# Kernel tuning notes

Hardware: AMD Instinct MI355X
Metric: run time of the kernel (lower is better)

Reference implementation:

```python
import jax, jax.numpy as jnp
import numpy as np
import math

# Config: 8 packed images, each a 32x32 patch grid (t=1) -> equal seglen 1024
NSEG, GH, GW = 8, 32, 32
L = GH * GW            # 1024 tokens per segment
S = NSEG * L           # 8192 packed tokens
H, NH = 1024, 16
HD = H // NH           # 64, head dim (rope dim), divisible by 4
MLP = 4096
THETA = 10000.0


def _make_rope_cos_sin():
    # Rope2DPosEmb._precompute_freqs_cis for a (GH, GW) grid, dim=HD
    flat = np.arange(L, dtype=np.float32)
    x_pos = flat % GW
    y_pos = flat // GW
    dim_range = np.arange(0, HD, 4, dtype=np.float32)[: HD // 4]
    freqs = 1.0 / THETA ** (dim_range / HD)          # [HD//4]
    x_f = np.outer(x_pos, freqs)                     # [L, HD//4]
    y_f = np.outer(y_pos, freqs)
    # interleave x/y angles per frequency -> [L, HD//2]
    ang = np.stack([x_f, y_f], axis=-1).reshape(L, HD // 2)
    ang = np.tile(ang, (NSEG, 1))                    # same grid repeated per image
    return jnp.asarray(np.cos(ang)), jnp.asarray(np.sin(ang))


def setup_inputs() -> dict:
    key = jax.random.key(0)
    ks = jax.random.split(key, 8)
    cos, sin = _make_rope_cos_sin()
    inp = {
        "x": jax.random.normal(ks[0], (S, H), jnp.float32),
        "wqkv": jax.random.normal(ks[1], (3 * H, H), jnp.float32) * math.sqrt(1.0 / H),
        "wo": jax.random.normal(ks[2], (H, H), jnp.float32) * math.sqrt(1.0 / H),
        "ln0_g": jnp.ones((H,), jnp.float32),
        "ln0_b": jnp.zeros((H,), jnp.float32),
        "ln1_g": jnp.ones((H,), jnp.float32),
        "ln1_b": jnp.zeros((H,), jnp.float32),
        "fc0_w": jax.random.normal(ks[3], (MLP, H), jnp.float32) * math.sqrt(2.0 / H),
        "fc0_b": jnp.zeros((MLP,), jnp.float32),
        "fc1_w": jax.random.normal(ks[4], (H, MLP), jnp.float32) * math.sqrt(2.0 / MLP),
        "fc1_b": jnp.zeros((H,), jnp.float32),
        "rope_cos": cos,
        "rope_sin": sin,
        "cu_seqlens": jnp.arange(NSEG + 1, dtype=jnp.int32) * L,
    }
    return inp


def _layernorm(x, g, b, eps=1e-5):
    m = x.mean(-1, keepdims=True)
    v = ((x - m) ** 2).mean(-1, keepdims=True)
    return (x - m) * jax.lax.rsqrt(v + eps) * g + b


def _apply_rope(x, cos, sin):
    # x: [S, NH, HD]; cos/sin: [S, HD//2]. Complex mult on (even, odd) pairs.
    xr = x.reshape(S, NH, HD // 2, 2)
    x0, x1 = xr[..., 0], xr[..., 1]
    c = cos[:, None, :]
    s = sin[:, None, :]
    o0 = x0 * c - x1 * s
    o1 = x0 * s + x1 * c
    return jnp.stack([o0, o1], axis=-1).reshape(S, NH, HD)


def reference(x, wqkv, wo, ln0_g, ln0_b, ln1_g, ln1_b,
              fc0_w, fc0_b, fc1_w, fc1_b, rope_cos, rope_sin, cu_seqlens):
    # --- attention branch (pre-norm) ---
    h = _layernorm(x, ln0_g, ln0_b)
    qkv = (h @ wqkv.T).reshape(S, 3, NH, HD)
    q, k, v = qkv[:, 0], qkv[:, 1], qkv[:, 2]
    q = _apply_rope(q, rope_cos, rope_sin)
    k = _apply_rope(k, rope_cos, rope_sin)
    # block-diagonal varlen attention: equal-length segments -> reshape
    qb = q.reshape(NSEG, L, NH, HD)
    kb = k.reshape(NSEG, L, NH, HD)
    vb = v.reshape(NSEG, L, NH, HD)
    scores = jnp.einsum("blhd,bmhd->bhlm", qb, kb) / math.sqrt(HD)
    p = jax.nn.softmax(scores.astype(jnp.float32), axis=-1).astype(x.dtype)
    attn = jnp.einsum("bhlm,bmhd->blhd", p, vb).reshape(S, H)
    x = x + attn @ wo.T
    # --- MLP branch (pre-norm) ---
    h2 = _layernorm(x, ln1_g, ln1_b)
    mlp = jax.nn.gelu(h2 @ fc0_w.T + fc0_b, approximate=False) @ fc1_w.T + fc1_b
    return x + mlp
```

## Files before the change

kernel.cpp:

```cpp
#include <hip/hip_runtime.h>
#include <math.h>


typedef __bf16 bf16x8 __attribute__((ext_vector_type(8)));
typedef float f32x4 __attribute__((ext_vector_type(4)));
typedef float f32x16 __attribute__((ext_vector_type(16)));
typedef unsigned int u32;

__device__ __forceinline__ unsigned short f2b(float f) {
  unsigned u = __float_as_uint(f);
  return (unsigned short)((u + 0x7FFFu + ((u >> 16) & 1u)) >> 16);
}
__device__ __forceinline__ float b2f(unsigned short h) {
  return __uint_as_float(((unsigned)h) << 16);
}
__device__ __forceinline__ void async_ld16(const void* g, void* l) {
  __builtin_amdgcn_global_load_lds((__attribute__((address_space(1))) void*)g,
                                   (__attribute__((address_space(3))) void*)l,
                                   16, 0, 0);
}
__device__ __forceinline__ float exp2fast(float x) {
#if __has_builtin(__builtin_amdgcn_exp2f)
  return __builtin_amdgcn_exp2f(x);
#else
  return exp2f(x);
#endif
}
__device__ __forceinline__ float rcpfast(float x) {
#if __has_builtin(__builtin_amdgcn_rcpf)
  return __builtin_amdgcn_rcpf(x);
#else
  return 1.0f / x;
#endif
}

__global__ __launch_bounds__(256) void castln_kernel(
    const float* __restrict__ w0, const float* __restrict__ w1,
    const float* __restrict__ w2, const float* __restrict__ w3,
    unsigned short* __restrict__ wdst,
    const float* __restrict__ x, const float* __restrict__ g,
    const float* __restrict__ bt, unsigned short* __restrict__ hout) {
  __shared__ float red[8];
  const int blk = blockIdx.x;
  if (blk < 12288) {
    const int t = blk * 256 + threadIdx.x;
    const float* src;
    int off;
    if (t < 786432) { src = w0; off = t; }
    else if (t < 1048576) { src = w1; off = t - 786432; }
    else if (t < 2097152) { src = w2; off = t - 1048576; }
    else { src = w3; off = t - 2097152; }
    const float4 v = ((const float4*)src)[off];
    ushort4 o;
    o.x = f2b(v.x); o.y = f2b(v.y); o.z = f2b(v.z); o.w = f2b(v.w);
    ((ushort4*)wdst)[t] = o;
    return;
  }
  const int row = blk - 12288, t = threadIdx.x;
  const float4 v = ((const float4*)(x + (size_t)row * 1024))[t];
  float s = v.x + v.y + v.z + v.w;
  float s2 = v.x * v.x + v.y * v.y + v.z * v.z + v.w * v.w;
#pragma unroll
  for (int m = 1; m < 64; m <<= 1) {
    s += __shfl_xor(s, m, 64);
    s2 += __shfl_xor(s2, m, 64);
  }
  if ((t & 63) == 0) { red[t >> 6] = s; red[4 + (t >> 6)] = s2; }
  __syncthreads();
  const float ts = red[0] + red[1] + red[2] + red[3];
  const float ts2 = red[4] + red[5] + red[6] + red[7];
  const float mean = ts * (1.f / 1024.f);
  const float var = ts2 * (1.f / 1024.f) - mean * mean;
  const float inv = rsqrtf(var + 1e-5f);
  const float4 gv = ((const float4*)g)[t];
  const float4 bv = ((const float4*)bt)[t];
  ushort4 o;
  o.x = f2b((v.x - mean) * inv * gv.x + bv.x);
  o.y = f2b((v.y - mean) * inv * gv.y + bv.y);
  o.z = f2b((v.z - mean) * inv * gv.z + bv.z);
  o.w = f2b((v.w - mean) * inv * gv.w + bv.w);
  ((ushort4*)hout)[(size_t)row * 256 + t] = o;
}

__global__ __launch_bounds__(256) void ln_kernel(const float* __restrict__ x,
                                                 const float* __restrict__ g,
                                                 const float* __restrict__ bt,
                                                 unsigned short* __restrict__ out) {
  __shared__ float red[8];
  const int row = blockIdx.x, t = threadIdx.x;
  const float4 v = ((const float4*)(x + (size_t)row * 1024))[t];
  float s = v.x + v.y + v.z + v.w;
  float s2 = v.x * v.x + v.y * v.y + v.z * v.z + v.w * v.w;
#pragma unroll
  for (int m = 1; m < 64; m <<= 1) {
    s += __shfl_xor(s, m, 64);
    s2 += __shfl_xor(s2, m, 64);
  }
  if ((t & 63) == 0) { red[t >> 6] = s; red[4 + (t >> 6)] = s2; }
  __syncthreads();
  const float ts = red[0] + red[1] + red[2] + red[3];
  const float ts2 = red[4] + red[5] + red[6] + red[7];
  const float mean = ts * (1.f / 1024.f);
  const float var = ts2 * (1.f / 1024.f) - mean * mean;
  const float inv = rsqrtf(var + 1e-5f);
  const float4 gv = ((const float4*)g)[t];
  const float4 bv = ((const float4*)bt)[t];
  ushort4 o;
  o.x = f2b((v.x - mean) * inv * gv.x + bv.x);
  o.y = f2b((v.y - mean) * inv * gv.y + bv.y);
  o.z = f2b((v.z - mean) * inv * gv.z + bv.z);
  o.w = f2b((v.w - mean) * inv * gv.w + bv.w);
  ((ushort4*)out)[(size_t)row * 256 + t] = o;
}

template <int MODE, int NBN, int BM>
__global__ __launch_bounds__(512, 2) void gemm_p8(
    const unsigned short* __restrict__ A, const unsigned short* __restrict__ B,
    int M, int N, int K, float* __restrict__ outf, unsigned short* __restrict__ outb,
    const float* __restrict__ res, const float* __restrict__ bias) {
  constexpr int NPH = (BM == 256) ? 4 : 2;
  constexpr int NF = (BM == 256) ? 2 : 4;
  constexpr int M_REP = BM / 32;
  constexpr int AI = BM / 128;
  constexpr int VST = AI + 2;
  constexpr int STG2 = (BM == 256) ? 2 : 1;
  __shared__ __align__(16) unsigned short As[2][2][BM * 32];
  __shared__ __align__(16) unsigned short Bs[2][2][256 * 32];
  const int bid = blockIdx.x;
  const int j8 = bid & 7, g = bid >> 3;
  const int bm = ((g / NBN) * 8 + j8) * BM;
  const int bn = (g % NBN) * 256;
  const int t = threadIdx.x, wave = t >> 6, lane = t & 63;
  const int quad = lane >> 4, l16 = lane & 15;
  const int wm = (wave >> 2) * (M_REP * 16);
  const int wn = (wave & 3) * 64;
  const int r16 = lane >> 2;
  const int cs8 = (((lane & 3) ^ ((lane >> 3) & 3)) * 8);
  const unsigned short* AgS[AI];
  unsigned short* AlS[AI];
#pragma unroll
  for (int i = 0; i < AI; i++) {
    const int r0 = wave * (AI * 16) + i * 16;
    AgS[i] = A + (size_t)(bm + r0 + r16) * K + cs8;
    AlS[i] = &As[0][0][r0 * 32];
  }
  const unsigned short* BgS[2];
  unsigned short* BlS[2];
#pragma unroll
  for (int i = 0; i < 2; i++) {
    const int r0 = wave * 32 + i * 16;
    BgS[i] = B + (size_t)(bn + r0 + r16) * K + cs8;
    BlS[i] = &Bs[0][0][r0 * 32];
  }
#define STG(bi, kt, ks)                                                      \
  do {                                                                       \
    _Pragma("unroll") for (int i_ = 0; i_ < AI; i_++)                        \
        async_ld16(AgS[i_] + (size_t)(kt) * 64 + (ks) * 32,                  \
                   AlS[i_] + ((bi) * 2 + (ks)) * (BM * 32));                 \
    _Pragma("unroll") for (int i_ = 0; i_ < 2; i_++)                         \
        async_ld16(BgS[i_] + (size_t)(kt) * 64 + (ks) * 32,                  \
                   BlS[i_] + ((bi) * 2 + (ks)) * (256 * 32));                \
  } while (0)

  f32x4 acc[M_REP][4] = {};
  const int NT = K >> 6;
  const int rq = ((quad ^ ((l16 >> 1) & 3)) * 8);
  STG(0, 0, 0);
  STG(0, 0, 1);
  STG(1, 1, 0);
  __builtin_amdgcn_sched_barrier(0);
  if (BM == 256) asm volatile("s_waitcnt vmcnt(4)" ::: "memory");
  else           asm volatile("s_waitcnt vmcnt(3)" ::: "memory");
  __builtin_amdgcn_sched_barrier(0);
  __builtin_amdgcn_s_barrier();
  __builtin_amdgcn_sched_barrier(0);

  bf16x8 af[M_REP];
  for (int u = 0; u < NT; ++u) {
    const int buf = u & 1, nbuf = buf ^ 1;
#pragma unroll
    for (int p = 0; p < NPH; ++p) {
      const int ks = (NPH == 4) ? (p >> 1) : p;
      const int j0 = (NPH == 4) ? (p & 1) * 2 : 0;
      const unsigned short* Ab = &As[buf][ks][0];
      const unsigned short* Bb = &Bs[buf][ks][0];
      if (NPH == 2 || (p & 1) == 0) {
#pragma unroll
        for (int i = 0; i < M_REP; i++)
          af[i] = *(const bf16x8*)(Ab + (wm + i * 16 + l16) * 32 + rq);
      }
      bf16x8 bfv[NF];
#pragma unroll
      for (int jj = 0; jj < NF; jj++)
        bfv[jj] = *(const bf16x8*)(Bb + (wn + (j0 + jj) * 16 + l16) * 32 + rq);
      if (p == 0 && u + 1 < NT) STG(nbuf, u + 1, 1);
      if (p == STG2 && u + 2 < NT) STG(buf, u + 2, 0);
      __builtin_amdgcn_sched_barrier(0);
      __builtin_amdgcn_s_barrier();
      asm volatile("s_waitcnt lgkmcnt(0)" ::: "memory");
      __builtin_amdgcn_sched_barrier(0);
      __builtin_amdgcn_s_setprio(1);
#pragma unroll
      for (int jj = 0; jj < NF; jj++)
#pragma unroll
        for (int i = 0; i < M_REP; i++)
          acc[i][j0 + jj] = __builtin_amdgcn_mfma_f32_16x16x32_bf16(
              af[i], bfv[jj], acc[i][j0 + jj], 0, 0, 0);
      __builtin_amdgcn_s_setprio(0);
      if (p == NPH - 1 && u + 1 < NT) {
        __builtin_amdgcn_sched_barrier(0);
        if (u + 2 < NT) {
          if (BM == 256) asm volatile("s_waitcnt vmcnt(4)" ::: "memory");
          else           asm volatile("s_waitcnt vmcnt(3)" ::: "memory");
        } else {
          asm volatile("s_waitcnt vmcnt(0)" ::: "memory");
        }
      }
      __builtin_amdgcn_sched_barrier(0);
      __builtin_amdgcn_s_barrier();
      __builtin_amdgcn_sched_barrier(0);
    }
  }
#undef STG
#pragma unroll
  for (int i = 0; i < M_REP; i++)
#pragma unroll
    for (int jj = 0; jj < 4; jj++)
#pragma unroll
      for (int r = 0; r < 4; r++) {
        const int m = bm + wm + i * 16 + quad * 4 + r;
        const int n = bn + wn + jj * 16 + l16;
        const size_t idx = (size_t)m * N + n;
        const float v = acc[i][jj][r];
        if (MODE == 1) {
          outf[idx] = v + res[idx];
        } else if (MODE == 2) {
          const float z = v + bias[n];
          const float u = z * (0.7978845608f + 0.03567740814f * z * z);
          const float e = fminf(u * 2.885390082f, 80.f);
          const float tt = exp2fast(e);
          outb[idx] = f2b(z * tt * rcpfast(tt + 1.0f));
        } else if (MODE == 3) {
          outf[idx] = v + bias[n] + res[idx];
        } else {
          outb[idx] = f2b(v);
        }
      }
}

__device__ __forceinline__ u32 rope2(u32 in, float c, float sn, float sc) {
  const float a = b2f((unsigned short)(in & 0xffff));
  const float b = b2f((unsigned short)(in >> 16));
  return (u32)f2b((a * c - b * sn) * sc) | ((u32)f2b((a * sn + b * c) * sc) << 16);
}
__global__ __launch_bounds__(256) void ropevt_kernel(const unsigned short* __restrict__ qkv,
                                                     const float* __restrict__ cb,
                                                     const float* __restrict__ sb,
                                                     unsigned short* __restrict__ qh,
                                                     unsigned short* __restrict__ kh,
                                                     unsigned short* __restrict__ vt) {
  __shared__ unsigned short tile[64][72];
  const int blk = blockIdx.x;
  if (blk < 4096) {
    const int tid = blk * 256 + threadIdx.x;
    const int ii = tid & 7, head = (tid >> 3) & 15, s = tid >> 7;
    const float4 cv = *(const float4*)(cb + s * 32 + ii * 4);
    const float4 sv = *(const float4*)(sb + s * 32 + ii * 4);
    const unsigned short* base = qkv + (size_t)s * 3072 + head * 64 + ii * 8;
    const uint4 qa = *(const uint4*)base;
    const uint4 ka = *(const uint4*)(base + 1024);
    const int seg = s >> 10, l = s & 1023;
    const size_t o = ((size_t)((seg * 16 + head) * 1024 + l)) * 64 + ii * 8;
    const float QSC = 0.125f * 1.44269504f;
    uint4 qo, ko;
    qo.x = rope2(qa.x, cv.x, sv.x, QSC); ko.x = rope2(ka.x, cv.x, sv.x, 1.f);
    qo.y = rope2(qa.y, cv.y, sv.y, QSC); ko.y = rope2(ka.y, cv.y, sv.y, 1.f);
    qo.z = rope2(qa.z, cv.z, sv.z, QSC); ko.z = rope2(ka.z, cv.z, sv.z, 1.f);
    qo.w = rope2(qa.w, cv.w, sv.w, QSC); ko.w = rope2(ka.w, cv.w, sv.w, 1.f);
    *(uint4*)(qh + o) = qo;
    *(uint4*)(kh + o) = ko;
    return;
  }
  const int b = blk - 4096;
  const int lt = b & 15, head = (b >> 4) & 15, seg = b >> 8;
  const int t = threadIdx.x;
  const int r = t >> 2, c0 = (t & 3) * 16;
  const unsigned short* src =
      qkv + ((size_t)(seg * 1024 + lt * 64 + r)) * 3072 + 2048 + head * 64 + c0;
#pragma unroll
  for (int k = 0; k < 16; k++) tile[r][c0 + k] = src[k];
  __syncthreads();
  unsigned short* dst =
      vt + ((size_t)((seg * 16 + head) * 64 + r)) * 1024 + lt * 64 + c0;
#pragma unroll
  for (int k = 0; k < 16; k++) dst[k] = tile[c0 + k][r];
}

__global__ __launch_bounds__(256) void attn_kernel(const unsigned short* __restrict__ qh,
                                                   const unsigned short* __restrict__ kh,
                                                   const unsigned short* __restrict__ vt,
                                                   unsigned short* __restrict__ out) {
  __shared__ __align__(16) unsigned short Qs[128 * 64];
  __shared__ __align__(16) unsigned short Ks[64 * 64];
  __shared__ __align__(16) unsigned short Vs[64 * 64];
  __shared__ float wl[128];
  const int b = blockIdx.x;
  const int head = b & 15, seg = (b >> 4) & 7, qt = b >> 7;
  const int t = threadIdx.x, wave = t >> 6, lane = t & 63;
  const int h = lane >> 5, q31 = lane & 31;
  const size_t sh = (size_t)(seg * 16 + head);
  const unsigned short* qbase = qh + (sh * 1024 + (size_t)qt * 128) * 64;
  const unsigned short* kbase = kh + sh * 1024 * 64;
  const unsigned short* vbase = vt + sh * 64 * 1024;
  const int r8 = lane >> 3;
  const int c8 = ((lane & 7) ^ (r8 & 7)) * 8;
#pragma unroll
  for (int cc = 0; cc < 4; cc++) {
    const int chunk = wave * 4 + cc;
    async_ld16(qbase + (size_t)(chunk * 8 + r8) * 64 + c8, Qs + chunk * 512);
  }
  const int qrow_l = wave * 32 + q31;
  const int qsw = qrow_l & 7;
  bf16x8 qf[4];
  float lsum = 0.f;
  f32x16 oacc[2] = {};

  for (int kt = 0; kt < 16; kt++) {
    const int ch0 = wave * 2;
    async_ld16(kbase + (size_t)(kt * 64 + ch0 * 8 + r8) * 64 + c8, Ks + ch0 * 512);
    async_ld16(kbase + (size_t)(kt * 64 + ch0 * 8 + 8 + r8) * 64 + c8, Ks + ch0 * 512 + 512);
    async_ld16(vbase + (size_t)(ch0 * 8 + r8) * 1024 + kt * 64 + c8, Vs + ch0 * 512);
    async_ld16(vbase + (size_t)(ch0 * 8 + 8 + r8) * 1024 + kt * 64 + c8, Vs + ch0 * 512 + 512);
    __syncthreads();
    if (kt == 0) {
#pragma unroll
      for (int ks = 0; ks < 4; ks++)
        qf[ks] = *(const bf16x8*)(Qs + qrow_l * 64 + (((2 * ks + h) ^ qsw)) * 8);
    }
    f32x16 st[2] = {{}, {}};
#pragma unroll
    for (int T = 0; T < 2; T++) {
      const int krow = 32 * T + q31;
      const int ksw = krow & 7;
#pragma unroll
      for (int ks = 0; ks < 4; ks++) {
        const bf16x8 kf = *(const bf16x8*)(Ks + krow * 64 + (((2 * ks + h) ^ ksw)) * 8);
        st[T] = __builtin_amdgcn_mfma_f32_32x32x16_bf16(kf, qf[ks], st[T], 0, 0, 0);
      }
    }
    u32 pk[2][4][2];
#pragma unroll
    for (int T = 0; T < 2; T++)
#pragma unroll
      for (int g = 0; g < 4; g++)
#pragma unroll
        for (int e = 0; e < 2; e++) {
          const float plo = exp2fast(st[T][4 * g + 2 * e]);
          const float phi = exp2fast(st[T][4 * g + 2 * e + 1]);
          lsum += plo + phi;
          pk[T][g][e] = (u32)f2b(plo) | ((u32)f2b(phi) << 16);
        }
    u32 rcv[2][4];
#pragma unroll
    for (int T = 0; T < 2; T++) {
      const u32 p0 = h ? pk[T][0][0] : pk[T][1][0];
      const u32 p1 = h ? pk[T][0][1] : pk[T][1][1];
      const u32 p2 = h ? pk[T][2][0] : pk[T][3][0];
      const u32 p3 = h ? pk[T][2][1] : pk[T][3][1];
      rcv[T][0] = (u32)__shfl_xor((int)p0, 32, 64);
      rcv[T][1] = (u32)__shfl_xor((int)p1, 32, 64);
      rcv[T][2] = (u32)__shfl_xor((int)p2, 32, 64);
      rcv[T][3] = (u32)__shfl_xor((int)p3, 32, 64);
    }
#pragma unroll
    for (int tt = 0; tt < 4; tt++) {
      const int T = tt >> 1, uu = tt & 1;
      union { u32 u[4]; bf16x8 v; } af;
      if (h == 0) {
        af.u[0] = pk[T][2 * uu][0];
        af.u[1] = pk[T][2 * uu][1];
        af.u[2] = rcv[T][2 * uu];
        af.u[3] = rcv[T][2 * uu + 1];
      } else {
        af.u[0] = rcv[T][2 * uu];
        af.u[1] = rcv[T][2 * uu + 1];
        af.u[2] = pk[T][2 * uu + 1][0];
        af.u[3] = pk[T][2 * uu + 1][1];
      }
#pragma unroll
      for (int ot = 0; ot < 2; ot++) {
        const int vrow = 32 * ot + q31;
        const int vsw = vrow & 7;
        const bf16x8 bv = *(const bf16x8*)(Vs + vrow * 64 + (((2 * tt + h) ^ vsw)) * 8);
        oacc[ot] = __builtin_amdgcn_mfma_f32_32x32x16_bf16(af.v, bv, oacc[ot], 0, 0, 0);
      }
    }
    __syncthreads();
  }
  lsum += __shfl_xor(lsum, 32, 64);
  if (h == 0) wl[wave * 32 + q31] = lsum;
  const int qglob = seg * 1024 + qt * 128 + wave * 32;
#pragma unroll
  for (int g = 0; g < 4; g++) {
    const float4 lv = *(const float4*)&wl[wave * 32 + 8 * g + 4 * h];
#pragma unroll
    for (int m = 0; m < 4; m++) {
      const int r16 = 4 * g + m;
      const int qrow = qglob + m + 8 * g + 4 * h;
      const float invl = rcpfast((&lv.x)[m]);
#pragma unroll
      for (int ot = 0; ot < 2; ot++)
        out[(size_t)qrow * 1024 + head * 64 + 32 * ot + q31] = f2b(oacc[ot][r16] * invl);
    }
  }
}

extern "C" void kernel_launch(void* const* d_in, const int* in_sizes, int n_in,
                              void* d_out, int out_size, void* d_ws, size_t ws_size,
                              hipStream_t stream) {
  (void)in_sizes; (void)n_in; (void)out_size; (void)ws_size;
  const float* x    = (const float*)d_in[0];
  const float* wqkv = (const float*)d_in[1];
  const float* wo   = (const float*)d_in[2];
  const float* ln0g = (const float*)d_in[3];
  const float* ln0b = (const float*)d_in[4];
  const float* ln1g = (const float*)d_in[5];
  const float* ln1b = (const float*)d_in[6];
  const float* fc0w = (const float*)d_in[7];
  const float* fc0b = (const float*)d_in[8];
  const float* fc1w = (const float*)d_in[9];
  const float* fc1b = (const float*)d_in[10];
  const float* rc   = (const float*)d_in[11];
  const float* rsn  = (const float*)d_in[12];
  float* out = (float*)d_out;
  char* w = (char*)d_ws;
  const size_t MB = 1u << 20;
  unsigned short* hb    = (unsigned short*)(w + 0);
  unsigned short* bqkv  = (unsigned short*)(w + 16 * MB);
  unsigned short* bwo   = (unsigned short*)(w + 22 * MB);
  unsigned short* bfc0  = (unsigned short*)(w + 24 * MB);
  unsigned short* bfc1  = (unsigned short*)(w + 32 * MB);
  unsigned short* qhb   = (unsigned short*)(w + 40 * MB);
  unsigned short* khb   = (unsigned short*)(w + 56 * MB);
  unsigned short* vtb   = (unsigned short*)(w + 72 * MB);
  unsigned short* attnb = (unsigned short*)(w + 88 * MB);
  unsigned short* qkvb  = (unsigned short*)(w + 104 * MB);
  unsigned short* midb  = (unsigned short*)(w + 104 * MB);

  castln_kernel<<<20480, 256, 0, stream>>>(wqkv, wo, fc0w, fc1w, bqkv,
                                           x, ln0g, ln0b, hb);
  gemm_p8<4, 12, 256><<<384, 512, 0, stream>>>(hb, bqkv, 8192, 3072, 1024,
                                               nullptr, qkvb, nullptr, nullptr);
  ropevt_kernel<<<6144, 256, 0, stream>>>(qkvb, rc, rsn, qhb, khb, vtb);
  attn_kernel<<<1024, 256, 0, stream>>>(qhb, khb, vtb, attnb);
  gemm_p8<1, 4, 128><<<256, 512, 0, stream>>>(attnb, bwo, 8192, 1024, 1024,
                                              out, nullptr, x, nullptr);
  ln_kernel<<<8192, 256, 0, stream>>>(out, ln1g, ln1b, hb);
  gemm_p8<2, 16, 256><<<512, 512, 0, stream>>>(hb, bfc0, 8192, 4096, 1024,
                                               nullptr, midb, nullptr, fc0b);
  gemm_p8<3, 4, 128><<<256, 512, 0, stream>>>(midb, bfc1, 8192, 1024, 4096,
                                              out, nullptr, out, fc1b);
}
```

Measured before the change: 492.9 us.

## Add double-buffered BK=64 GEMM kernel for fc0 with XOR-swizzled LDS

```diff
diff --git a/kernel.cpp b/kernel.cpp
--- a/kernel.cpp
+++ b/kernel.cpp
@@ -122,7 +122,6 @@
   constexpr int NF = (BM == 256) ? 2 : 4;
   constexpr int M_REP = BM / 32;
   constexpr int AI = BM / 128;
-  constexpr int VST = AI + 2;
   constexpr int STG2 = (BM == 256) ? 2 : 1;
   __shared__ __align__(16) unsigned short As[2][2][BM * 32];
   __shared__ __align__(16) unsigned short Bs[2][2][256 * 32];
@@ -232,6 +231,130 @@
         const int n = bn + wn + jj * 16 + l16;
         const size_t idx = (size_t)m * N + n;
         const float v = acc[i][jj][r];
+        if (MODE == 1) {
+          outf[idx] = v + res[idx];
+        } else if (MODE == 2) {
+          const float z = v + bias[n];
+          const float u = z * (0.7978845608f + 0.03567740814f * z * z);
+          const float e = fminf(u * 2.885390082f, 80.f);
+          const float tt = exp2fast(e);
+          outb[idx] = f2b(z * tt * rcpfast(tt + 1.0f));
+        } else if (MODE == 3) {
+          outf[idx] = v + bias[n] + res[idx];
+        } else {
+          outb[idx] = f2b(v);
+        }
+      }
+}
+
+template <int MODE, int NBN, int BN>
+__global__ __launch_bounds__(512, 2) void gemm_bt8(
+    const unsigned short* __restrict__ A, const unsigned short* __restrict__ B,
+    int M, int N, int K, float* __restrict__ outf, unsigned short* __restrict__ outb,
+    const float* __restrict__ res, const float* __restrict__ bias) {
+  constexpr int NBI = BN / 64;
+  constexpr int WN_WAVES = BN / 64;
+  constexpr int WM_WAVES = 8 / WN_WAVES;
+  constexpr int M_REP = (256 / WM_WAVES) / 16;
+  constexpr int N_REP = 4;
+  __shared__ __align__(16) unsigned short As[2][256 * 64];
+  __shared__ __align__(16) unsigned short Bs[2][BN * 64];
+  const int bid = blockIdx.x;
+  const int j8 = bid & 7, g = bid >> 3;
+  const int bm = ((g / NBN) * 8 + j8) * 256;
+  const int bn = (g % NBN) * BN;
+  const int t = threadIdx.x, wave = t >> 6, lane = t & 63;
+  const int quad = lane >> 4, l16 = lane & 15;
+  const int wm = (wave / WN_WAVES) * (M_REP * 16);
+  const int wn = (wave % WN_WAVES) * 64;
+  const int l8 = lane >> 3;
+  const int cs = ((lane & 7) ^ (l8 & 7)) * 8;
+  const unsigned short* Ag[4];
+  unsigned short* Al[4];
+#pragma unroll
+  for (int i = 0; i < 4; i++) {
+    const int r = wave * 32 + i * 8;
+    Ag[i] = A + (size_t)(bm + r + l8) * K + cs;
+    Al[i] = &As[0][r * 64];
+  }
+  const unsigned short* Bg[NBI];
+  unsigned short* Bl[NBI];
+#pragma unroll
+  for (int i = 0; i < NBI; i++) {
+    const int r = wave * (NBI * 8) + i * 8;
+    Bg[i] = B + (size_t)(bn + r + l8) * K + cs;
+    Bl[i] = &Bs[0][r * 64];
+  }
+#define STAGE(bi, k0)                                                        \
+  do {                                                                       \
+    _Pragma("unroll") for (int i_ = 0; i_ < 4; i_++)                         \
+        async_ld16(Ag[i_] + (k0), Al[i_] + (bi) * (256 * 64));               \
+    _Pragma("unroll") for (int i_ = 0; i_ < NBI; i_++)                       \
+        async_ld16(Bg[i_] + (k0), Bl[i_] + (bi) * (BN * 64));                \
+  } while (0)
+
+  f32x4 acc[M_REP][N_REP] = {};
+  const int NT = K >> 6;
+  const int swk = l16 & 7;
+  STAGE(0, 0);
+  STAGE(1, 64);
+  if (BN == 256) asm volatile("s_waitcnt vmcnt(8)" ::: "memory");
+  else           asm volatile("s_waitcnt vmcnt(6)" ::: "memory");
+  __builtin_amdgcn_sched_barrier(0);
+  __builtin_amdgcn_s_barrier();
+  __builtin_amdgcn_sched_barrier(0);
+  int k0 = 128;
+  for (int tI = 0; tI < NT; ++tI) {
+    const int cur = tI & 1;
+    const unsigned short* Ab = &As[cur][0];
+    const unsigned short* Bb = &Bs[cur][0];
+#pragma unroll
+    for (int ks = 0; ks < 2; ks++) {
+      bf16x8 af[M_REP], bfv[N_REP];
+#pragma unroll
+      for (int i = 0; i < M_REP; i++)
+        af[i] = *(const bf16x8*)(Ab + (wm + i * 16 + l16) * 64 +
+                                 (((ks * 4 + quad) ^ swk) * 8));
+#pragma unroll
+      for (int j = 0; j < N_REP; j++)
+        bfv[j] = *(const bf16x8*)(Bb + (wn + j * 16 + l16) * 64 +
+                                  (((ks * 4 + quad) ^ swk) * 8));
+      __builtin_amdgcn_s_setprio(1);
+#pragma unroll
+      for (int j = 0; j < N_REP; j++)
+#pragma unroll
+        for (int i = 0; i < M_REP; i++)
+          acc[i][j] = __builtin_amdgcn_mfma_f32_16x16x32_bf16(af[i], bfv[j],
+                                                              acc[i][j], 0, 0, 0);
+      __builtin_amdgcn_s_setprio(0);
+    }
+    if (tI + 1 == NT) break;
+    __builtin_amdgcn_sched_barrier(0);
+    __builtin_amdgcn_s_barrier();
+    __builtin_amdgcn_sched_barrier(0);
+    if (tI + 2 < NT) {
+      STAGE(cur, k0);
+      k0 += 64;
+      if (BN == 256) asm volatile("s_waitcnt vmcnt(8)" ::: "memory");
+      else           asm volatile("s_waitcnt vmcnt(6)" ::: "memory");
+    } else {
+      asm volatile("s_waitcnt vmcnt(0)" ::: "memory");
+    }
+    __builtin_amdgcn_sched_barrier(0);
+    __builtin_amdgcn_s_barrier();
+    __builtin_amdgcn_sched_barrier(0);
+  }
+#undef STAGE
+#pragma unroll
+  for (int i = 0; i < M_REP; i++)
+#pragma unroll
+    for (int j = 0; j < N_REP; j++)
+#pragma unroll
+      for (int r = 0; r < 4; r++) {
+        const int m = bm + wm + i * 16 + quad * 4 + r;
+        const int n = bn + wn + j * 16 + l16;
+        const size_t idx = (size_t)m * N + n;
+        const float v = acc[i][j][r];
         if (MODE == 1) {
           outf[idx] = v + res[idx];
         } else if (MODE == 2) {
@@ -456,8 +579,8 @@
   gemm_p8<1, 4, 128><<<256, 512, 0, stream>>>(attnb, bwo, 8192, 1024, 1024,
                                               out, nullptr, x, nullptr);
   ln_kernel<<<8192, 256, 0, stream>>>(out, ln1g, ln1b, hb);
-  gemm_p8<2, 16, 256><<<512, 512, 0, stream>>>(hb, bfc0, 8192, 4096, 1024,
-                                               nullptr, midb, nullptr, fc0b);
+  gemm_bt8<2, 16, 256><<<512, 512, 0, stream>>>(hb, bfc0, 8192, 4096, 1024,
+                                                nullptr, midb, nullptr, fc0b);
   gemm_p8<3, 4, 128><<<256, 512, 0, stream>>>(midb, bfc1, 8192, 1024, 4096,
                                               out, nullptr, out, fc1b);
 }
```

New measurement: 490.7 us. No clear change (-0.4%).

## Add barrier-free per-wave staged GEMM kernel for the fc0 GELU projection

Applied to the files above, without the earlier changes.

```diff
diff --git a/kernel.cpp b/kernel.cpp
--- a/kernel.cpp
+++ b/kernel.cpp
@@ -122,7 +122,6 @@
   constexpr int NF = (BM == 256) ? 2 : 4;
   constexpr int M_REP = BM / 32;
   constexpr int AI = BM / 128;
-  constexpr int VST = AI + 2;
   constexpr int STG2 = (BM == 256) ? 2 : 1;
   __shared__ __align__(16) unsigned short As[2][2][BM * 32];
   __shared__ __align__(16) unsigned short Bs[2][2][256 * 32];
@@ -240,6 +239,101 @@
           const float e = fminf(u * 2.885390082f, 80.f);
           const float tt = exp2fast(e);
           outb[idx] = f2b(z * tt * rcpfast(tt + 1.0f));
+        } else if (MODE == 3) {
+          outf[idx] = v + bias[n] + res[idx];
+        } else {
+          outb[idx] = f2b(v);
+        }
+      }
+}
+
+template <int MODE, int NBN>
+__global__ __launch_bounds__(256, 2) void gemm_pw(
+    const unsigned short* __restrict__ A, const unsigned short* __restrict__ B,
+    int M, int N, int K, float* __restrict__ outf, unsigned short* __restrict__ outb,
+    const float* __restrict__ res, const float* __restrict__ bias) {
+  __shared__ __align__(16) unsigned short L[4 * 8192];
+  const int bid = blockIdx.x;
+  const int j8 = bid & 7, g = bid >> 3;
+  const int bm = ((g / NBN) * 8 + j8) * 128;
+  const int bn = (g % NBN) * 128;
+  const int t = threadIdx.x, wave = t >> 6, lane = t & 63;
+  const int quad = lane >> 4, l16 = lane & 15;
+  const int wm = (wave >> 1) * 64, wn = (wave & 1) * 64;
+  const int r16 = lane >> 2;
+  const int cs8 = (((lane & 3) ^ ((lane >> 3) & 3)) * 8);
+  const unsigned short* Ag[4];
+  const unsigned short* Bg[4];
+#pragma unroll
+  for (int i = 0; i < 4; i++) {
+    Ag[i] = A + (size_t)(bm + wm + i * 16 + r16) * K + cs8;
+    Bg[i] = B + (size_t)(bn + wn + i * 16 + r16) * K + cs8;
+  }
+  unsigned short* Wb = L + wave * 8192;
+#define STG(tt, bi)                                                          \
+  do {                                                                       \
+    const size_t ko_ = (size_t)(tt) * 32;                                    \
+    _Pragma("unroll") for (int i_ = 0; i_ < 4; i_++) {                       \
+      async_ld16(Ag[i_] + ko_, Wb + (bi) * 4096 + i_ * 512);                 \
+      async_ld16(Bg[i_] + ko_, Wb + (bi) * 4096 + 2048 + i_ * 512);          \
+    }                                                                        \
+  } while (0)
+  f32x4 acc[4][4] = {};
+  const int NT = K >> 5;
+  const int swg = (l16 >> 1) & 3;
+  STG(0, 0);
+  STG(1, 1);
+  asm volatile("s_waitcnt vmcnt(8)" ::: "memory");
+  __builtin_amdgcn_sched_barrier(0);
+  for (int tt = 0; tt < NT; ++tt) {
+    const int cur = tt & 1;
+    const unsigned short* Ab = Wb + cur * 4096;
+    const unsigned short* Bb = Ab + 2048;
+    bf16x8 af[4], bfv[4];
+#pragma unroll
+    for (int i = 0; i < 4; i++)
+      af[i] = *(const bf16x8*)(Ab + (i * 16 + l16) * 32 + (quad ^ swg) * 8);
+#pragma unroll
+    for (int j = 0; j < 4; j++)
+      bfv[j] = *(const bf16x8*)(Bb + (j * 16 + l16) * 32 + (quad ^ swg) * 8);
+    asm volatile("s_waitcnt lgkmcnt(0)" ::: "memory");
+    __builtin_amdgcn_sched_barrier(0);
+    if (tt + 2 < NT) STG(tt + 2, cur);
+    __builtin_amdgcn_sched_barrier(0);
+    __builtin_amdgcn_s_setprio(1);
+#pragma unroll
+    for (int j = 0; j < 4; j++)
+#pragma unroll
+      for (int i = 0; i < 4; i++)
+        acc[i][j] = __builtin_amdgcn_mfma_f32_16x16x32_bf16(af[i], bfv[j],
+                                                            acc[i][j], 0, 0, 0);
+    __builtin_amdgcn_s_setprio(0);
+    if (tt + 1 < NT) {
+      __builtin_amdgcn_sched_barrier(0);
+      if (tt + 2 < NT) asm volatile("s_waitcnt vmcnt(8)" ::: "memory");
+      else             asm volatile("s_waitcnt vmcnt(0)" ::: "memory");
+      __builtin_amdgcn_sched_barrier(0);
+    }
+  }
+#undef STG
+#pragma unroll
+  for (int i = 0; i < 4; i++)
+#pragma unroll
+    for (int jj = 0; jj < 4; jj++)
+#pragma unroll
+      for (int r = 0; r < 4; r++) {
+        const int m = bm + wm + i * 16 + quad * 4 + r;
+        const int n = bn + wn + jj * 16 + l16;
+        const size_t idx = (size_t)m * N + n;
+        const float v = acc[i][jj][r];
+        if (MODE == 1) {
+          outf[idx] = v + res[idx];
+        } else if (MODE == 2) {
+          const float z = v + bias[n];
+          const float u = z * (0.7978845608f + 0.03567740814f * z * z);
+          const float e = fminf(u * 2.885390082f, 80.f);
+          const float tt2 = exp2fast(e);
+          outb[idx] = f2b(z * tt2 * rcpfast(tt2 + 1.0f));
         } else if (MODE == 3) {
           outf[idx] = v + bias[n] + res[idx];
         } else {
@@ -456,8 +550,8 @@
   gemm_p8<1, 4, 128><<<256, 512, 0, stream>>>(attnb, bwo, 8192, 1024, 1024,
                                               out, nullptr, x, nullptr);
   ln_kernel<<<8192, 256, 0, stream>>>(out, ln1g, ln1b, hb);
-  gemm_p8<2, 16, 256><<<512, 512, 0, stream>>>(hb, bfc0, 8192, 4096, 1024,
-                                               nullptr, midb, nullptr, fc0b);
+  gemm_pw<2, 32><<<2048, 256, 0, stream>>>(hb, bfc0, 8192, 4096, 1024,
+                                           nullptr, midb, nullptr, fc0b);
   gemm_p8<3, 4, 128><<<256, 512, 0, stream>>>(midb, bfc1, 8192, 1024, 4096,
                                               out, nullptr, out, fc1b);
 }
```

New measurement: 550.8 us. 11.7% more time.
